# Kernel tuning notes

Hardware: AMD Instinct MI355X
Metric: run time of the kernel (lower is better)

The kernel has to match this reference:

```python
import jax, jax.numpy as jnp
import numpy as np

TEMPERATURE = 1.0

def setup_inputs() -> dict:
    key = jax.random.key(0)
    k1, k2, k3 = jax.random.split(key, 3)
    B, N, D = 1024, 256, 512
    return {
        "fg_img_feature": jax.random.normal(k1, (B, D), dtype=jnp.float32),
        "fg_pro_feature": jax.random.normal(k2, (B, D), dtype=jnp.float32),
        "bg_pro_feature": jax.random.normal(k3, (B, N, D), dtype=jnp.float32),
    }

def reference(fg_img_feature, fg_pro_feature, bg_pro_feature):
    # Only the image features are L2-normalized (matches original module).
    img = fg_img_feature / jnp.linalg.norm(fg_img_feature, axis=-1, keepdims=True)  # [B, D]
    # Per-sample scalar logit: img_i . fg_pro_i
    pos_logits = jnp.sum(img * fg_pro_feature, axis=-1) / TEMPERATURE  # [B]
    # Per-sample batched matvec against N background prototypes.
    bg_logits = jnp.einsum('bd,bnd->bn', img, bg_pro_feature) / TEMPERATURE  # [B, N]
    positive_sims = jnp.sum(jnp.exp(pos_logits))
    negative_sims = positive_sims + jnp.sum(jnp.exp(bg_logits))
    return -jnp.log(positive_sims / negative_sims)
```

## Files before the change

kernel.cpp:

```cpp
#include <hip/hip_runtime.h>
#include <hip/hip_bf16.h>
#include <math.h>


#define D_DIM   512
#define NSPLIT  16
#define ROWS_PER_WAVE 4

__global__ __launch_bounds__(256, 4) void infonce_main(
    const float* __restrict__ img,
    const float* __restrict__ fg_pro,
    const float* __restrict__ bg_pro,
    float* __restrict__ part_out,
    int N, int B)
{
    const int bid   = blockIdx.x;
    const int b     = bid >> 4;
    const int split = bid & 15;
    const int tid   = threadIdx.x;
    const int wid   = tid >> 6;
    const int lane  = tid & 63;

    __shared__ float s_img[D_DIM];
    __shared__ float s_red[8];

    const float2 v = reinterpret_cast<const float2*>(img + (size_t)b * D_DIM)[tid];
    float ss = v.x * v.x + v.y * v.y;
    #pragma unroll
    for (int off = 32; off > 0; off >>= 1) ss += __shfl_xor(ss, off);
    if (lane == 0) s_red[wid] = ss;
    __syncthreads();
    const float inv = rsqrtf(s_red[0] + s_red[1] + s_red[2] + s_red[3]);

    const float2 nv = make_float2(v.x * inv, v.y * inv);
    reinterpret_cast<float2*>(s_img)[tid] = nv;

    if (split == 0) {
        const float2 p = reinterpret_cast<const float2*>(fg_pro + (size_t)b * D_DIM)[tid];
        float pd = nv.x * p.x + nv.y * p.y;
        #pragma unroll
        for (int off = 32; off > 0; off >>= 1) pd += __shfl_xor(pd, off);
        if (lane == 0) s_red[4 + wid] = pd;
    }
    __syncthreads();
    if (split == 0 && tid == 0) {
        const float pos = s_red[4] + s_red[5] + s_red[6] + s_red[7];
        part_out[(size_t)B * NSPLIT + b] = expf(pos);
    }

    const int n0 = split * (N / NSPLIT) + wid * ROWS_PER_WAVE;

    const float4* s_img4 = reinterpret_cast<const float4*>(s_img);
    const float4  a0 = s_img4[lane];
    const float4  a1 = s_img4[64 + lane];

    const float4* bg4 = reinterpret_cast<const float4*>(
        bg_pro + (size_t)b * N * D_DIM + (size_t)n0 * D_DIM);

    const float4* r0 = bg4;
    const float4* r1 = bg4 + 1 * (D_DIM / 4);
    const float4* r2 = bg4 + 2 * (D_DIM / 4);
    const float4* r3 = bg4 + 3 * (D_DIM / 4);
    const float4 b00 = r0[lane], b01 = r0[64 + lane];
    const float4 b10 = r1[lane], b11 = r1[64 + lane];
    const float4 b20 = r2[lane], b21 = r2[64 + lane];
    const float4 b30 = r3[lane], b31 = r3[64 + lane];

    float d0 = a0.x*b00.x + a0.y*b00.y + a0.z*b00.z + a0.w*b00.w
             + a1.x*b01.x + a1.y*b01.y + a1.z*b01.z + a1.w*b01.w;
    float d1 = a0.x*b10.x + a0.y*b10.y + a0.z*b10.z + a0.w*b10.w
             + a1.x*b11.x + a1.y*b11.y + a1.z*b11.z + a1.w*b11.w;
    float d2 = a0.x*b20.x + a0.y*b20.y + a0.z*b20.z + a0.w*b20.w
             + a1.x*b21.x + a1.y*b21.y + a1.z*b21.z + a1.w*b21.w;
    float d3 = a0.x*b30.x + a0.y*b30.y + a0.z*b30.z + a0.w*b30.w
             + a1.x*b31.x + a1.y*b31.y + a1.z*b31.z + a1.w*b31.w;

    #pragma unroll
    for (int off = 32; off > 0; off >>= 1) {
        d0 += __shfl_xor(d0, off);
        d1 += __shfl_xor(d1, off);
        d2 += __shfl_xor(d2, off);
        d3 += __shfl_xor(d3, off);
    }
    if (lane == 0)
        s_red[wid] = expf(d0) + expf(d1) + expf(d2) + expf(d3);
    __syncthreads();
    if (tid == 0)
        part_out[bid] = s_red[0] + s_red[1] + s_red[2] + s_red[3];
}

__global__ __launch_bounds__(256) void infonce_finalize(
    const float* __restrict__ part, float* __restrict__ out,
    int nneg, int npos)
{
    const int tid = threadIdx.x;
    float neg = 0.0f, pos = 0.0f;
    for (int i = tid; i < nneg; i += 256) neg += part[i];
    for (int i = tid; i < npos; i += 256) pos += part[nneg + i];
    #pragma unroll
    for (int off = 32; off > 0; off >>= 1) {
        neg += __shfl_xor(neg, off);
        pos += __shfl_xor(pos, off);
    }
    __shared__ float sn[4], sp[4];
    if ((tid & 63) == 0) { sn[tid >> 6] = neg; sp[tid >> 6] = pos; }
    __syncthreads();
    if (tid == 0) {
        const float P = sp[0] + sp[1] + sp[2] + sp[3];
        const float Ntot = sn[0] + sn[1] + sn[2] + sn[3];
        out[0] = logf(P + Ntot) - logf(P);
    }
}

extern "C" void kernel_launch(void* const* d_in, const int* in_sizes, int n_in,
                              void* d_out, int out_size, void* d_ws, size_t ws_size,
                              hipStream_t stream)
{
    const float* img = (const float*)d_in[0];
    const float* fg  = (const float*)d_in[1];
    const float* bg  = (const float*)d_in[2];
    float* out  = (float*)d_out;
    float* part = (float*)d_ws;

    const int B = in_sizes[0] / (D_DIM * (int)sizeof(float));
    const int N = in_sizes[2] / in_sizes[0];

    infonce_main<<<B * NSPLIT, 256, 0, stream>>>(img, fg, bg, part, N, B);
    infonce_finalize<<<1, 256, 0, stream>>>(part, out, B * NSPLIT, B);
}
```

Baseline: 600.0 us.

## Precompute normalized image rows and positive logits in a separate kernel

Adds a pre-pass kernel that L2-normalizes each image row once, writes it to workspace and computes the exponentiated positive logits. The main kernel then loads the already-normalized row from global memory. This drops the per-block norm reduction, the shared-memory staging and a barrier, none of which are repeated 16 times per row anymore. The cost is an extra kernel launch and a round-trip of the normalized rows through global memory, in a kernel whose main cost is streaming the background tensor.

```diff
diff --git a/kernel.cpp b/kernel.cpp
--- a/kernel.cpp
+++ b/kernel.cpp
@@ -7,12 +7,49 @@
 #define NSPLIT  16
 #define ROWS_PER_WAVE 4
 
-__global__ __launch_bounds__(256, 4) void infonce_main(
+__global__ __launch_bounds__(256) void infonce_norm(
     const float* __restrict__ img,
     const float* __restrict__ fg_pro,
+    float* __restrict__ img_norm,
+    float* __restrict__ pos_out,
+    int B)
+{
+    const int row  = blockIdx.x * 4 + (threadIdx.x >> 6);
+    const int lane = threadIdx.x & 63;
+    if (row >= B) return;
+
+    const float4* img4 = reinterpret_cast<const float4*>(img) + (size_t)row * (D_DIM / 4);
+    const float4 a0 = img4[lane];
+    const float4 a1 = img4[64 + lane];
+
+    float ss = a0.x*a0.x + a0.y*a0.y + a0.z*a0.z + a0.w*a0.w
+             + a1.x*a1.x + a1.y*a1.y + a1.z*a1.z + a1.w*a1.w;
+    #pragma unroll
+    for (int off = 32; off > 0; off >>= 1) ss += __shfl_xor(ss, off);
+    const float inv = rsqrtf(ss);
+
+    const float4 n0 = make_float4(a0.x*inv, a0.y*inv, a0.z*inv, a0.w*inv);
+    const float4 n1 = make_float4(a1.x*inv, a1.y*inv, a1.z*inv, a1.w*inv);
+
+    float4* out4 = reinterpret_cast<float4*>(img_norm) + (size_t)row * (D_DIM / 4);
+    out4[lane]      = n0;
+    out4[64 + lane] = n1;
+
+    const float4* fg4 = reinterpret_cast<const float4*>(fg_pro) + (size_t)row * (D_DIM / 4);
+    const float4 f0 = fg4[lane];
+    const float4 f1 = fg4[64 + lane];
+    float pd = n0.x*f0.x + n0.y*f0.y + n0.z*f0.z + n0.w*f0.w
+             + n1.x*f1.x + n1.y*f1.y + n1.z*f1.z + n1.w*f1.w;
+    #pragma unroll
+    for (int off = 32; off > 0; off >>= 1) pd += __shfl_xor(pd, off);
+    if (lane == 0) pos_out[row] = expf(pd);
+}
+
+__global__ __launch_bounds__(256, 4) void infonce_main(
+    const float* __restrict__ img_norm,
     const float* __restrict__ bg_pro,
-    float* __restrict__ part_out,
-    int N, int B)
+    float* __restrict__ neg_out,
+    int N)
 {
     const int bid   = blockIdx.x;
     const int b     = bid >> 4;
@@ -21,39 +58,11 @@
     const int wid   = tid >> 6;
     const int lane  = tid & 63;
 
-    __shared__ float s_img[D_DIM];
-    __shared__ float s_red[8];
-
-    const float2 v = reinterpret_cast<const float2*>(img + (size_t)b * D_DIM)[tid];
-    float ss = v.x * v.x + v.y * v.y;
-    #pragma unroll
-    for (int off = 32; off > 0; off >>= 1) ss += __shfl_xor(ss, off);
-    if (lane == 0) s_red[wid] = ss;
-    __syncthreads();
-    const float inv = rsqrtf(s_red[0] + s_red[1] + s_red[2] + s_red[3]);
-
-    const float2 nv = make_float2(v.x * inv, v.y * inv);
-    reinterpret_cast<float2*>(s_img)[tid] = nv;
-
-    if (split == 0) {
-        const float2 p = reinterpret_cast<const float2*>(fg_pro + (size_t)b * D_DIM)[tid];
-        float pd = nv.x * p.x + nv.y * p.y;
-        #pragma unroll
-        for (int off = 32; off > 0; off >>= 1) pd += __shfl_xor(pd, off);
-        if (lane == 0) s_red[4 + wid] = pd;
-    }
-    __syncthreads();
-    if (split == 0 && tid == 0) {
-        const float pos = s_red[4] + s_red[5] + s_red[6] + s_red[7];
-        part_out[(size_t)B * NSPLIT + b] = expf(pos);
-    }
+    const float4* in4 = reinterpret_cast<const float4*>(img_norm) + (size_t)b * (D_DIM / 4);
+    const float4 a0 = in4[lane];
+    const float4 a1 = in4[64 + lane];
 
     const int n0 = split * (N / NSPLIT) + wid * ROWS_PER_WAVE;
-
-    const float4* s_img4 = reinterpret_cast<const float4*>(s_img);
-    const float4  a0 = s_img4[lane];
-    const float4  a1 = s_img4[64 + lane];
-
     const float4* bg4 = reinterpret_cast<const float4*>(
         bg_pro + (size_t)b * N * D_DIM + (size_t)n0 * D_DIM);
 
@@ -82,11 +91,13 @@
         d2 += __shfl_xor(d2, off);
         d3 += __shfl_xor(d3, off);
     }
+
+    __shared__ float s_red[4];
     if (lane == 0)
         s_red[wid] = expf(d0) + expf(d1) + expf(d2) + expf(d3);
     __syncthreads();
     if (tid == 0)
-        part_out[bid] = s_red[0] + s_red[1] + s_red[2] + s_red[3];
+        neg_out[bid] = s_red[0] + s_red[1] + s_red[2] + s_red[3];
 }
 
 __global__ __launch_bounds__(256) void infonce_finalize(
@@ -119,12 +130,16 @@
     const float* img = (const float*)d_in[0];
     const float* fg  = (const float*)d_in[1];
     const float* bg  = (const float*)d_in[2];
-    float* out  = (float*)d_out;
-    float* part = (float*)d_ws;
+    float* out = (float*)d_out;
 
     const int B = in_sizes[0] / (D_DIM * (int)sizeof(float));
     const int N = in_sizes[2] / in_sizes[0];
 
-    infonce_main<<<B * NSPLIT, 256, 0, stream>>>(img, fg, bg, part, N, B);
-    infonce_finalize<<<1, 256, 0, stream>>>(part, out, B * NSPLIT, B);
+    float* neg      = (float*)d_ws;
+    float* pos      = neg + (size_t)B * NSPLIT;
+    float* img_norm = pos + B;
+
+    infonce_norm<<<B / 4, 256, 0, stream>>>(img, fg, img_norm, pos, B);
+    infonce_main<<<B * NSPLIT, 256, 0, stream>>>(img_norm, bg, neg, N);
+    infonce_finalize<<<1, 256, 0, stream>>>(neg, out, B * NSPLIT, B);
 }
```

Measured after the change: 600.1 us. Within noise of the previous version (+0.0%).
